# Kernel optimization log

Measured on AMD Instinct MI355X. Metric: run time of the kernel, lower is better.

Reference implementation:

```python
import jax, jax.numpy as jnp
import numpy as np
from jax.scipy.special import erfc

# Constants baked into PmeModule.__init__ (NNPOps PME)
GRID = (14, 15, 16)          # reciprocal mesh
ORDER = 5                    # B-spline order
ALPHA = 4.985823141035867    # Ewald splitting parameter (1/nm)
COULOMB = 138.935            # ONE_4PI_EPS0, kJ/mol*nm/e^2
CUTOFF = 0.5                 # direct-space cutoff (forward arg in source)
N_ATOMS = 4096


def _M(k, x):
    """Cardinal B-spline M_k evaluated elementwise (Essmann et al. 1995)."""
    if k == 1:
        return jnp.where((x >= 0.0) & (x < 1.0), 1.0, 0.0)
    return (x * _M(k - 1, x) + (k - x) * _M(k - 1, x - 1.0)) / (k - 1)


def _bspline_moduli(K):
    """|b(m)|^2 per axis; zero out ill-defined modes (odd order, m=K/2)."""
    m = jnp.arange(K)
    kk = jnp.arange(ORDER - 1, dtype=jnp.float32)
    Mv = _M(ORDER, kk + 1.0)                                   # M_n(1..n-1)
    ph = jnp.exp(2j * jnp.pi * m[:, None] * kk[None, :] / K)
    denom = (Mv[None, :] * ph).sum(-1)
    d2 = jnp.abs(denom) ** 2
    return jnp.where(d2 < 1e-7, 0.0, 1.0 / d2)


def _direct(positions, charges, box):
    # All-pairs minimum-image (triclinic-reduced) erfc/r sum within cutoff.
    delta = positions[:, None, :] - positions[None, :, :]      # [N,N,3]
    for a in (2, 1, 0):
        delta = delta - box[a] * jnp.round(delta[..., a:a + 1] / box[a, a])
    r2 = (delta ** 2).sum(-1)                                  # [N,N]
    n = positions.shape[0]
    mask = (r2 < CUTOFF ** 2) & ~jnp.eye(n, dtype=bool)
    r = jnp.sqrt(jnp.where(mask, r2, 1.0))
    qq = charges[:, None] * charges[None, :]
    e = jnp.where(mask, qq * erfc(ALPHA * r) / r, 0.0)
    return 0.5 * COULOMB * e.sum()                             # each pair once


def _spread(positions, charges, box):
    """Spread charges onto the mesh with order-5 B-splines (periodic)."""
    frac = positions @ jnp.linalg.inv(box)                     # fractional coords
    frac = frac - jnp.floor(frac)                              # wrap to [0,1)
    u = frac * jnp.array(GRID, jnp.float32)                    # [N,3]
    base = jnp.floor(u)
    w = u - base
    offs = jnp.arange(ORDER, dtype=jnp.float32)
    wts = _M(ORDER, w[:, :, None] + offs[None, None, :])       # [N,3,ORDER]
    idx = (base.astype(jnp.int32)[:, :, None]
           - jnp.arange(ORDER, dtype=jnp.int32)[None, None, :]) \
          % jnp.array(GRID, jnp.int32)[None, :, None]          # [N,3,ORDER]
    wq = (charges[:, None, None, None] * wts[:, 0, :, None, None]
          * wts[:, 1, None, :, None] * wts[:, 2, None, None, :])  # [N,5,5,5]
    fi = (idx[:, 0, :, None, None] * (GRID[1] * GRID[2])
          + idx[:, 1, None, :, None] * GRID[2]
          + idx[:, 2, None, None, :])                          # flat indices
    g = jnp.zeros(GRID[0] * GRID[1] * GRID[2], positions.dtype)
    return g.at[fi.reshape(-1)].add(wq.reshape(-1)).reshape(GRID)


def _reciprocal(positions, charges, box):
    Q = _spread(positions, charges, box)
    F = jnp.fft.fftn(Q)
    recip = jnp.linalg.inv(box)                                # recip vecs = columns
    mx = jnp.fft.fftfreq(GRID[0]) * GRID[0]
    my = jnp.fft.fftfreq(GRID[1]) * GRID[1]
    mz = jnp.fft.fftfreq(GRID[2]) * GRID[2]
    mv = (mx[:, None, None, None] * recip.T[0]
          + my[None, :, None, None] * recip.T[1]
          + mz[None, None, :, None] * recip.T[2])              # [Kx,Ky,Kz,3]
    m2 = (mv ** 2).sum(-1)
    B = (_bspline_moduli(GRID[0])[:, None, None]
         * _bspline_moduli(GRID[1])[None, :, None]
         * _bspline_moduli(GRID[2])[None, None, :])
    nz = m2 > 0.0
    m2s = jnp.where(nz, m2, 1.0)
    green = jnp.where(nz, jnp.exp(-(jnp.pi ** 2) * m2s / ALPHA ** 2) / m2s, 0.0)
    V = jnp.abs(jnp.linalg.det(box))
    erec = COULOMB / (2.0 * jnp.pi * V) * (green * B * jnp.abs(F) ** 2).sum()
    eself = -COULOMB * ALPHA / jnp.sqrt(jnp.pi) * (charges ** 2).sum()
    return erec + eself


def setup_inputs() -> dict:
    key = jax.random.key(0)
    k1, k2 = jax.random.split(key)
    box = jnp.diag(jnp.array([3.0, 3.1, 3.2], jnp.float32))    # nm, diagonal box
    positions = jax.random.uniform(k1, (N_ATOMS, 3), jnp.float32) * jnp.diag(box)
    charges = 0.5 * jax.random.normal(k2, (N_ATOMS,), jnp.float32)
    return {"positions": positions, "charges": charges, "box_vectors": box}


def reference(positions, charges, box_vectors):
    edir = _direct(positions, charges, box_vectors)
    erecip = _reciprocal(positions, charges, box_vectors)
    return edir - erecip
```

## Files before the change

### kernel.cpp

```cpp
#include <hip/hip_runtime.h>
#include <math.h>

#define NATOM 4096
#define KX 14
#define KY 15
#define KZ 16
#define SLAB (KY*KZ)
#define NGRID (KX*SLAB)
#define NB 128
#define APB (NATOM/NB)
#define NTRI 544

static constexpr float ALPHA_F   = 4.985823141035867f;
static constexpr float COULOMB_F = 138.935f;
static constexpr float CUT2_F    = 0.25f;
static constexpr float TWOPI_F   = 6.283185307179586f;
static constexpr float PI_F      = 3.14159265358979f;

#define POIS32 0xAAAAAAAAu
#define CTR_LAST (POIS32 + 15u)

__device__ __forceinline__ float M1f(float x){ return (x >= 0.f && x < 1.f) ? 1.f : 0.f; }
__device__ __forceinline__ float M2f(float x){ return x*M1f(x) + (2.f-x)*M1f(x-1.f); }
__device__ __forceinline__ float M3f(float x){ return (x*M2f(x) + (3.f-x)*M2f(x-1.f)) * 0.5f; }
__device__ __forceinline__ float M4f(float x){ return (x*M3f(x) + (4.f-x)*M3f(x-1.f)) * (1.f/3.f); }
__device__ __forceinline__ float M5f(float x){ return (x*M4f(x) + (5.f-x)*M4f(x-1.f)) * 0.25f; }

__device__ __forceinline__ void inv3x3(const float* b, float* inv){
  float det = b[0]*(b[4]*b[8]-b[5]*b[7]) - b[1]*(b[3]*b[8]-b[5]*b[6]) + b[2]*(b[3]*b[7]-b[4]*b[6]);
  float id = 1.f/det;
  inv[0] = (b[4]*b[8]-b[5]*b[7])*id;
  inv[1] = (b[2]*b[7]-b[1]*b[8])*id;
  inv[2] = (b[1]*b[5]-b[2]*b[4])*id;
  inv[3] = (b[5]*b[6]-b[3]*b[8])*id;
  inv[4] = (b[0]*b[8]-b[2]*b[6])*id;
  inv[5] = (b[2]*b[3]-b[0]*b[5])*id;
  inv[6] = (b[3]*b[7]-b[4]*b[6])*id;
  inv[7] = (b[1]*b[6]-b[0]*b[7])*id;
  inv[8] = (b[0]*b[4]-b[1]*b[3])*id;
}

__device__ __forceinline__ float bmod(int m, int K){
  float base = TWOPI_F * (float)m / (float)K;
  float s, c;
  float dr = 1.f/24.f, di = 0.f;
  __sincosf(base,      &s, &c); dr += (11.f/24.f)*c; di += (11.f/24.f)*s;
  __sincosf(base*2.f,  &s, &c); dr += (11.f/24.f)*c; di += (11.f/24.f)*s;
  __sincosf(base*3.f,  &s, &c); dr += (1.f/24.f)*c;  di += (1.f/24.f)*s;
  float d2 = dr*dr + di*di;
  return (d2 < 1e-7f) ? 0.f : 1.f/d2;
}

__device__ __forceinline__ float erfc_poly(float x){
  float tt = __builtin_amdgcn_rcpf(1.f + 0.3275911f*x);
  return ((((1.061405429f*tt - 1.453152027f)*tt + 1.421413741f)*tt
          - 0.284496736f)*tt + 0.254829592f)*tt;
}

__global__ __launch_bounds__(256) void fat_kernel(const float* __restrict__ pos,
    const float* __restrict__ chg, const float* __restrict__ box,
    float* __restrict__ grid, double* __restrict__ dpart)
{
  __shared__ float sg[NGRID];
  __shared__ float sx[64], sy[64], sz[64], sw[64];
  __shared__ double red4[4];
  int t = threadIdx.x;
  int b = blockIdx.x;

  if (b < NTRI){
    int rem = b, ci = 0;
    while (true){ int cnt = 64 - 4*ci; if (rem < cnt) break; rem -= cnt; ++ci; }
    int cj = 4*ci + rem;
    bool offdiag = (rem >= 4);
    int i  = ci*256 + t;
    int j0 = cj*64;
    if (t < 64){
      int j = j0 + t;
      sx[t] = pos[j*3+0]; sy[t] = pos[j*3+1]; sz[t] = pos[j*3+2]; sw[t] = chg[j];
    }
    __syncthreads();

    float b00=box[0],b01=box[1],b02=box[2],
          b10=box[3],b11=box[4],b12=box[5],
          b20=box[6],b21=box[7],b22=box[8];
    bool diag = (b01==0.f && b02==0.f && b10==0.f && b12==0.f && b20==0.f && b21==0.f);
    float i00 = 1.f/b00, i11 = 1.f/b11, i22 = 1.f/b22;

    float xi = pos[i*3+0], yi = pos[i*3+1], zi = pos[i*3+2], qi = chg[i];
    const float A2 = ALPHA_F*ALPHA_F;
    float e = 0.f;

    if (diag){
      #pragma unroll 4
      for (int jj = 0; jj < 64; ++jj){
        float dx = xi - sx[jj], dy = yi - sy[jj], dz = zi - sz[jj];
        dz -= b22*rintf(dz*i22);
        dy -= b11*rintf(dy*i11);
        dx -= b00*rintf(dx*i00);
        float r2 = dx*dx + dy*dy + dz*dz;
        if (r2 < CUT2_F && (j0 + jj) != i){
          float rinv = __builtin_amdgcn_rsqf(r2);
          float x = ALPHA_F * (r2 * rinv);
          e += qi * sw[jj] * erfc_poly(x) * __expf(-A2*r2) * rinv;
        }
      }
    } else {
      for (int jj = 0; jj < 64; ++jj){
        float dx = xi - sx[jj], dy = yi - sy[jj], dz = zi - sz[jj];
        float t2 = rintf(dz * i22); dx -= b20*t2; dy -= b21*t2; dz -= b22*t2;
        float t1 = rintf(dy * i11); dx -= b10*t1; dy -= b11*t1; dz -= b12*t1;
        float t0 = rintf(dx * i00); dx -= b00*t0; dy -= b01*t0; dz -= b02*t0;
        float r2 = dx*dx + dy*dy + dz*dz;
        if (r2 < CUT2_F && (j0 + jj) != i){
          float rinv = __builtin_amdgcn_rsqf(r2);
          float x = ALPHA_F * (r2 * rinv);
          e += qi * sw[jj] * erfc_poly(x) * __expf(-A2*r2) * rinv;
        }
      }
    }

    double de = (double)e;
    #pragma unroll
    for (int off = 32; off > 0; off >>= 1) de += __shfl_down(de, off);
    if ((t & 63) == 0) red4[t >> 6] = de;
    __syncthreads();
    if (t == 0){
      double s = red4[0]+red4[1]+red4[2]+red4[3];
      dpart[b] = offdiag ? 2.0*s : s;
    }

  } else {
    int sb = b - NTRI;
    for (int i = t; i < NGRID; i += 256) sg[i] = 0.f;
    __syncthreads();

    if (t < APB*5){
      int a   = t / 5;
      int jxi = t - 5*a;
      int atom = sb*APB + a;
      float bx[9], inv[9];
      #pragma unroll
      for (int i = 0; i < 9; ++i) bx[i] = box[i];
      inv3x3(bx, inv);

      float px = pos[atom*3+0], py = pos[atom*3+1], pz = pos[atom*3+2];
      float qi = chg[atom];
      float fr[3];
      fr[0] = px*inv[0] + py*inv[3] + pz*inv[6];
      fr[1] = px*inv[1] + py*inv[4] + pz*inv[7];
      fr[2] = px*inv[2] + py*inv[5] + pz*inv[8];

      const int Ks[3] = {KX, KY, KZ};
      float w[3][5]; int id[3][5];
      #pragma unroll
      for (int ax = 0; ax < 3; ++ax) {
        float f = fr[ax] - floorf(fr[ax]);
        float u = f * (float)Ks[ax];
        float bse = floorf(u);
        float x = u - bse;
        int bi = (int)bse;
        #pragma unroll
        for (int j = 0; j < 5; ++j) {
          w[ax][j] = M5f(x + (float)j);
          int ii = bi - j; if (ii < 0) ii += Ks[ax];
          id[ax][j] = ii;
        }
      }
      float qx = qi * w[0][jxi];
      int ox = id[0][jxi]*SLAB;
      #pragma unroll
      for (int jy = 0; jy < 5; ++jy) {
        float qxy = qx * w[1][jy];
        int oxy = ox + id[1][jy]*KZ;
        #pragma unroll
        for (int jz = 0; jz < 5; ++jz)
          atomicAdd(&sg[oxy + id[2][jz]], qxy * w[2][jz]);
      }
    }
    __syncthreads();
    for (int i = t; i < NGRID; i += 256){
      float v = sg[i];
      if (v != 0.f) atomicAdd(&grid[i], v);
    }
  }
}

__global__ __launch_bounds__(256) void recip_kernel(const float* __restrict__ grid,
    const float* __restrict__ chg, const float* __restrict__ box,
    const double* __restrict__ dpart, double* __restrict__ acc_rec,
    unsigned* __restrict__ ctr, float* __restrict__ out)
{
  __shared__ float2 Ty[KY*KY];
  __shared__ float2 Tx[KX*KX];
  __shared__ float2 Cz[KX*KY];
  __shared__ float2 Cyv[KX*KY];
  __shared__ double red[12];
  __shared__ int lastflag;
  int t  = threadIdx.x;
  int mz = blockIdx.x;
  const float P = __uint_as_float(POIS32);

  if (t < KY*KY){
    int my = t / KY, gy = t % KY;
    float s, c; __sincosf(-TWOPI_F*(float)((my*gy)%KY)/(float)KY, &s, &c);
    Ty[t] = make_float2(c, s);
  }
  if (t < KX*KX){
    int mx = t / KX, gx = t % KX;
    float s, c; __sincosf(-TWOPI_F*(float)((mx*gx)%KX)/(float)KX, &s, &c);
    Tx[t] = make_float2(c, s);
  }

  int u = t;
  if (u < KX*KY){
    const float4* g4 = (const float4*)grid;
    float q[16];
    #pragma unroll
    for (int k = 0; k < 4; ++k){
      float4 v = g4[u*4 + k];
      q[4*k+0] = v.x - P; q[4*k+1] = v.y - P; q[4*k+2] = v.z - P; q[4*k+3] = v.w - P;
    }
    float br = 0.f, bi = 0.f;
    #pragma unroll
    for (int gz = 0; gz < KZ; ++gz){
      float s, c; __sincosf(-TWOPI_F*(float)((mz*gz)%KZ)/(float)KZ, &s, &c);
      br += q[gz]*c; bi += q[gz]*s;
    }
    Cz[u] = make_float2(br, bi);
  }
  __syncthreads();

  if (u < KX*KY){
    int gx = u / KY, my = u % KY;
    float ar = 0.f, ai = 0.f;
    #pragma unroll
    for (int gy = 0; gy < KY; ++gy){
      float2 v = Cz[gx*KY + gy];
      float2 w = Ty[my*KY + gy];
      ar += v.x*w.x - v.y*w.y;
      ai += v.x*w.y + v.y*w.x;
    }
    Cyv[u] = make_float2(ar, ai);
  }
  __syncthreads();

  double s_rec = 0.0;
  if (u < KX*KY){
    int mx = u / KY, my = u % KY;
    float Fr = 0.f, Fi = 0.f;
    #pragma unroll
    for (int gx = 0; gx < KX; ++gx){
      float2 v = Cyv[gx*KY + my];
      float2 w = Tx[mx*KX + gx];
      Fr += v.x*w.x - v.y*w.y;
      Fi += v.x*w.y + v.y*w.x;
    }
    float bx[9], inv[9];
    #pragma unroll
    for (int k = 0; k < 9; ++k) bx[k] = box[k];
    inv3x3(bx, inv);
    float fx = (mx <= (KX-1)/2) ? (float)mx : (float)(mx - KX);
    float fy = (my <= (KY-1)/2) ? (float)my : (float)(my - KY);
    float fz = (mz <= (KZ-1)/2) ? (float)mz : (float)(mz - KZ);
    float mv0 = fx*inv[0] + fy*inv[1] + fz*inv[2];
    float mv1 = fx*inv[3] + fy*inv[4] + fz*inv[5];
    float mv2 = fx*inv[6] + fy*inv[7] + fz*inv[8];
    float m2 = mv0*mv0 + mv1*mv1 + mv2*mv2;
    float B  = bmod(mx,KX)*bmod(my,KY)*bmod(mz,KZ);
    if (m2 > 0.f && B > 0.f){
      float green = __expf(-(PI_F*PI_F)*m2/(ALPHA_F*ALPHA_F)) / m2;
      s_rec = (double)(green*B) * ((double)Fr*(double)Fr + (double)Fi*(double)Fi);
    }
  }

  #pragma unroll
  for (int off = 32; off > 0; off >>= 1) s_rec += __shfl_down(s_rec, off);
  int lane = t & 63, wid = t >> 6;
  if (lane == 0) red[wid] = s_rec;
  __syncthreads();
  if (t == 0){
    atomicAdd(acc_rec, red[0]+red[1]+red[2]+red[3]);
    asm volatile("s_waitcnt vmcnt(0)" ::: "memory");
    unsigned old = __hip_atomic_fetch_add(ctr, 1u, __ATOMIC_RELAXED, __HIP_MEMORY_SCOPE_AGENT);
    lastflag = (old == CTR_LAST) ? 1 : 0;
  }
  __syncthreads();

  if (lastflag){
    double s_dir = dpart[t] + dpart[t+256] + ((t < NTRI-512) ? dpart[t+512] : 0.0);
    double s_q2 = 0.0;
    #pragma unroll
    for (int i = t; i < NATOM; i += 256){ double q = (double)chg[i]; s_q2 += q*q; }
    #pragma unroll
    for (int off = 32; off > 0; off >>= 1){
      s_dir += __shfl_down(s_dir, off);
      s_q2  += __shfl_down(s_q2,  off);
    }
    if (lane == 0){ red[4+wid] = s_dir; red[8+wid] = s_q2; }
    __syncthreads();
    if (t == 0){
      double D = red[4]+red[5]+red[6]+red[7];
      double Q = red[8]+red[9]+red[10]+red[11];
      double R = __hip_atomic_load(acc_rec, __ATOMIC_ACQUIRE, __HIP_MEMORY_SCOPE_AGENT);
      double b00=box[0],b01=box[1],b02=box[2],
             b10=box[3],b11=box[4],b12=box[5],
             b20=box[6],b21=box[7],b22=box[8];
      double det = b00*(b11*b22 - b12*b21) - b01*(b10*b22 - b12*b20) + b02*(b10*b21 - b11*b20);
      double V = fabs(det);
      const double PI_D = 3.141592653589793238462643;
      double edir  = 0.5 * (double)COULOMB_F * D;
      double erec  = (double)COULOMB_F / (2.0*PI_D*V) * R;
      double eself = -(double)COULOMB_F * 4.985823141035867 / sqrt(PI_D) * Q;
      out[0] = (float)(edir - erec - eself);
    }
  }
}

extern "C" void kernel_launch(void* const* d_in, const int* in_sizes, int n_in,
                              void* d_out, int out_size, void* d_ws, size_t ws_size,
                              hipStream_t stream) {
  const float* pos = (const float*)d_in[0];
  const float* chg = (const float*)d_in[1];
  const float* box = (const float*)d_in[2];
  float* out = (float*)d_out;

  char* w = (char*)d_ws;
  float*    grid    = (float*)w;
  double*   dpart   = (double*)(w + 16384);
  double*   acc_rec = (double*)(w + 24576);
  unsigned* ctr     = (unsigned*)(w + 24584);

  fat_kernel<<<NTRI + NB, 256, 0, stream>>>(pos, chg, box, grid, dpart);
  recip_kernel<<<KZ, 256, 0, stream>>>(grid, chg, box, dpart, acc_rec, ctr, out);
}
```

Before: 78.00 us.

## Spread charges per grid column with direct writes instead of global atomics

The charge-spreading blocks no longer each build a full shared-memory mesh over a subset of atoms and atomically add it into global memory. Each block now owns one (x,y) column of the mesh, scans all atoms, accumulates only the atoms whose stencil touches that column into 16 shared z-bins, and writes the column directly. This drops the 3360-entry shared grid, the global atomics and the dependence on a poisoned or pre-zeroed global grid, so the poison subtraction in the reciprocal kernel goes away. In exchange every one of 210 blocks reads all 4096 atom positions and recomputes fractional coordinates, adding redundant global reads and arithmetic.

```diff
diff --git a/kernel.cpp b/kernel.cpp
--- a/kernel.cpp
+++ b/kernel.cpp
@@ -7,9 +7,8 @@
 #define KZ 16
 #define SLAB (KY*KZ)
 #define NGRID (KX*SLAB)
-#define NB 128
-#define APB (NATOM/NB)
 #define NTRI 544
+#define NCOL (KX*KY)
 
 static constexpr float ALPHA_F   = 4.985823141035867f;
 static constexpr float COULOMB_F = 138.935f;
@@ -61,9 +60,9 @@
     const float* __restrict__ chg, const float* __restrict__ box,
     float* __restrict__ grid, double* __restrict__ dpart)
 {
-  __shared__ float sg[NGRID];
   __shared__ float sx[64], sy[64], sz[64], sw[64];
   __shared__ double red4[4];
+  __shared__ float zacc[KZ];
   int t = threadIdx.x;
   int b = blockIdx.x;
 
@@ -130,58 +129,39 @@
     }
 
   } else {
-    int sb = b - NTRI;
-    for (int i = t; i < NGRID; i += 256) sg[i] = 0.f;
-    __syncthreads();
-
-    if (t < APB*5){
-      int a   = t / 5;
-      int jxi = t - 5*a;
-      int atom = sb*APB + a;
-      float bx[9], inv[9];
-      #pragma unroll
-      for (int i = 0; i < 9; ++i) bx[i] = box[i];
-      inv3x3(bx, inv);
-
-      float px = pos[atom*3+0], py = pos[atom*3+1], pz = pos[atom*3+2];
-      float qi = chg[atom];
-      float fr[3];
-      fr[0] = px*inv[0] + py*inv[3] + pz*inv[6];
-      fr[1] = px*inv[1] + py*inv[4] + pz*inv[7];
-      fr[2] = px*inv[2] + py*inv[5] + pz*inv[8];
-
-      const int Ks[3] = {KX, KY, KZ};
-      float w[3][5]; int id[3][5];
-      #pragma unroll
-      for (int ax = 0; ax < 3; ++ax) {
-        float f = fr[ax] - floorf(fr[ax]);
-        float u = f * (float)Ks[ax];
-        float bse = floorf(u);
-        float x = u - bse;
-        int bi = (int)bse;
+    int col = b - NTRI;
+    int gx = col / KY, gy = col % KY;
+    if (t < KZ) zacc[t] = 0.f;
+    __syncthreads();
+
+    float bx[9], inv[9];
+    #pragma unroll
+    for (int k = 0; k < 9; ++k) bx[k] = box[k];
+    inv3x3(bx, inv);
+
+    for (int a = t; a < NATOM; a += 256){
+      float px = pos[a*3+0], py = pos[a*3+1], pz = pos[a*3+2];
+      float f0 = px*inv[0] + py*inv[3] + pz*inv[6];
+      float f1 = px*inv[1] + py*inv[4] + pz*inv[7];
+      float f2 = px*inv[2] + py*inv[5] + pz*inv[8];
+      f0 -= floorf(f0); f1 -= floorf(f1); f2 -= floorf(f2);
+      float u0 = f0 * (float)KX, u1 = f1 * (float)KY, u2 = f2 * (float)KZ;
+      float bs0 = floorf(u0), bs1 = floorf(u1), bs2 = floorf(u2);
+      int bi0 = (int)bs0, bi1 = (int)bs1, bi2 = (int)bs2;
+      int jx = bi0 - gx; if (jx < 0) jx += KX;
+      int jy = bi1 - gy; if (jy < 0) jy += KY;
+      if (jx < 5 && jy < 5){
+        float x0 = u0 - bs0, x1 = u1 - bs1, x2 = u2 - bs2;
+        float qxy = chg[a] * M5f(x0 + (float)jx) * M5f(x1 + (float)jy);
         #pragma unroll
-        for (int j = 0; j < 5; ++j) {
-          w[ax][j] = M5f(x + (float)j);
-          int ii = bi - j; if (ii < 0) ii += Ks[ax];
-          id[ax][j] = ii;
+        for (int jz = 0; jz < 5; ++jz){
+          int iz = bi2 - jz; if (iz < 0) iz += KZ;
+          atomicAdd(&zacc[iz], qxy * M5f(x2 + (float)jz));
         }
       }
-      float qx = qi * w[0][jxi];
-      int ox = id[0][jxi]*SLAB;
-      #pragma unroll
-      for (int jy = 0; jy < 5; ++jy) {
-        float qxy = qx * w[1][jy];
-        int oxy = ox + id[1][jy]*KZ;
-        #pragma unroll
-        for (int jz = 0; jz < 5; ++jz)
-          atomicAdd(&sg[oxy + id[2][jz]], qxy * w[2][jz]);
-      }
-    }
-    __syncthreads();
-    for (int i = t; i < NGRID; i += 256){
-      float v = sg[i];
-      if (v != 0.f) atomicAdd(&grid[i], v);
-    }
+    }
+    __syncthreads();
+    if (t < KZ) grid[col*KZ + t] = zacc[t];
   }
 }
 
@@ -198,7 +178,6 @@
   __shared__ int lastflag;
   int t  = threadIdx.x;
   int mz = blockIdx.x;
-  const float P = __uint_as_float(POIS32);
 
   if (t < KY*KY){
     int my = t / KY, gy = t % KY;
@@ -218,7 +197,7 @@
     #pragma unroll
     for (int k = 0; k < 4; ++k){
       float4 v = g4[u*4 + k];
-      q[4*k+0] = v.x - P; q[4*k+1] = v.y - P; q[4*k+2] = v.z - P; q[4*k+3] = v.w - P;
+      q[4*k+0] = v.x; q[4*k+1] = v.y; q[4*k+2] = v.z; q[4*k+3] = v.w;
     }
     float br = 0.f, bi = 0.f;
     #pragma unroll
@@ -330,6 +309,6 @@
   double*   acc_rec = (double*)(w + 24576);
   unsigned* ctr     = (unsigned*)(w + 24584);
 
-  fat_kernel<<<NTRI + NB, 256, 0, stream>>>(pos, chg, box, grid, dpart);
+  fat_kernel<<<NTRI + NCOL, 256, 0, stream>>>(pos, chg, box, grid, dpart);
   recip_kernel<<<KZ, 256, 0, stream>>>(grid, chg, box, dpart, acc_rec, ctr, out);
 }
```

After: 85.88 us. 10.1% more time.
